# Performance work log

Hardware: AMD Instinct MI355X
Metric: run time of the kernel (lower is better)

Reference implementation:

```python
import jax, jax.numpy as jnp
import numpy as np

B = 16384

def setup_inputs() -> dict:
    key = jax.random.key(0)
    k1, k2, k3 = jax.random.split(key, 3)
    predictions = jax.random.uniform(k1, (B, 7 * 7 * 30), dtype=jnp.float32)
    targets = jax.random.uniform(k2, (B, 7 * 7 * 25), dtype=jnp.float32)
    # channel 4 of each grid cell is the object-present indicator, compared to exactly 1
    t = targets.reshape(B, 7, 7, 25)
    present = (jax.random.uniform(k3, (B, 7, 7)) > 0.5).astype(jnp.float32)
    t = t.at[..., 4].set(present)
    targets = t.reshape(B, 7 * 7 * 25)
    return {"predictions": predictions, "targets": targets}


def reference(predictions, targets):
    num_batches = predictions.shape[0]
    p = predictions.reshape(num_batches, 7, 7, 30)
    t = targets.reshape(num_batches, 7, 7, 25)

    c1 = p[..., 4]
    c2 = p[..., 9]
    c = t[..., 4]
    present = (c == 1.0)
    responsible1 = c1 > c2  # box 1 is responsible

    # objectiveness loss
    obj_present = jnp.where(responsible1, jnp.square(c1 - c), jnp.square(c2 - c))
    obj_absent = 0.5 * (jnp.square(c1) + jnp.square(c2))
    obj_loss = jnp.sum(jnp.where(present, obj_present, obj_absent))

    # classification loss (only where object present)
    cls_sq = jnp.sum(jnp.square(p[..., 10:30] - t[..., 5:25]), axis=-1)  # [B,7,7]
    class_loss = jnp.sum(jnp.where(present, cls_sq, 0.0))

    r = responsible1[..., None]
    p_center = jnp.where(r, p[..., 0:2], p[..., 5:7])
    p_hw = jnp.where(r, p[..., 2:4], p[..., 7:9])
    t_center = t[..., 0:2]
    t_hw = t[..., 2:4]
    box_sq = (jnp.sum(jnp.square(p_center - t_center), axis=-1)
              + jnp.sum(jnp.square(jnp.sqrt(p_hw) - jnp.sqrt(t_hw)), axis=-1))  # [B,7,7]
    box_loss = 5.0 * jnp.sum(jnp.where(present, box_sq, 0.0))

    return obj_loss + class_loss + box_loss
```

## Files before the change

kernel.cpp:

```cpp
#include <hip/hip_runtime.h>
#include <stdint.h>


#define TPB    64
#define KT     7
#define GRID   1792
#define P_F4   480
#define T_F4   400

#define GL2LDS(gptr, lptr)                                                    \
    __builtin_amdgcn_global_load_lds(                                         \
        (const __attribute__((address_space(1))) void*)(gptr),                \
        (__attribute__((address_space(3))) void*)(uintptr_t)(lptr), 16, 0, 0)

__global__ __launch_bounds__(TPB) void yolo_loss_kernel(
    const float* __restrict__ pred,
    const float* __restrict__ targ,
    float* __restrict__ out)
{
    __shared__ float4 spA[P_F4], stA[T_F4];
    __shared__ float4 spB[P_F4], stB[T_F4];

    const int tid = threadIdx.x;

    auto STAGE = [&](int t, float4* sp4, float4* st4) {
        const float4* gp = (const float4*)pred + (size_t)t * P_F4;
        const float4* gt = (const float4*)targ + (size_t)t * T_F4;
        #pragma unroll
        for (int r = 0; r < 7; ++r) GL2LDS(gp + tid + r * 64, sp4 + tid + r * 64);
        if (tid < 32)               GL2LDS(gp + 448 + tid,    sp4 + 448 + tid);
        #pragma unroll
        for (int r = 0; r < 6; ++r) GL2LDS(gt + tid + r * 64, st4 + tid + r * 64);
        if (tid < 16)               GL2LDS(gt + 384 + tid,    st4 + 384 + tid);
    };

    auto CELL = [&](const float* sp, const float* st) -> float {
        const float2* pv2 = (const float2*)(sp + tid * 30);
        float pv[30];
        #pragma unroll
        for (int i = 0; i < 15; ++i) {
            float2 v = pv2[i];
            pv[2*i] = v.x; pv[2*i+1] = v.y;
        }
        const float* tvp = st + tid * 25;
        float tv[25];
        #pragma unroll
        for (int i = 0; i < 25; ++i) tv[i] = tvp[i];

        float c1 = pv[4], c2 = pv[9], cc = tv[4];
        bool present = (cc == 1.0f);
        bool resp1   = (c1 > c2);

        float d1 = c1 - cc, d2 = c2 - cc;
        float obj = present ? (resp1 ? d1 * d1 : d2 * d2)
                            : 0.5f * (c1 * c1 + c2 * c2);

        float cls = 0.0f;
        #pragma unroll
        for (int k = 0; k < 20; ++k) {
            float d = pv[10 + k] - tv[5 + k];
            cls += d * d;
        }

        float pc0 = resp1 ? pv[0] : pv[5];
        float pc1 = resp1 ? pv[1] : pv[6];
        float ph0 = resp1 ? pv[2] : pv[7];
        float ph1 = resp1 ? pv[3] : pv[8];
        float b0 = pc0 - tv[0];
        float b1 = pc1 - tv[1];
        float s0 = sqrtf(ph0) - sqrtf(tv[2]);
        float s1 = sqrtf(ph1) - sqrtf(tv[3]);
        float box = b0 * b0 + b1 * b1 + s0 * s0 + s1 * s1;

        return obj + (present ? (cls + 5.0f * box) : 0.0f);
    };

    const int base = blockIdx.x * KT;
    float loss = 0.0f;

    STAGE(base, spA, stA);

    #pragma unroll
    for (int j = 0; j < KT; ++j) {
        const bool odd = (j & 1);
        if (j + 1 < KT) {
            if (odd) STAGE(base + j + 1, spA, stA);
            else     STAGE(base + j + 1, spB, stB);
            asm volatile("s_waitcnt vmcnt(15)" ::: "memory");
        } else {
            asm volatile("s_waitcnt vmcnt(0)" ::: "memory");
        }
        __builtin_amdgcn_sched_barrier(0);

        loss += odd ? CELL((const float*)spB, (const float*)stB)
                    : CELL((const float*)spA, (const float*)stA);
    }

    #pragma unroll
    for (int off = 32; off > 0; off >>= 1)
        loss += __shfl_down(loss, off);
    if (tid == 0)
        atomicAdd(out, loss);
}

extern "C" void kernel_launch(void* const* d_in, const int* in_sizes, int n_in,
                              void* d_out, int out_size, void* d_ws, size_t ws_size,
                              hipStream_t stream)
{
    const float* pred = (const float*)d_in[0];
    const float* targ = (const float*)d_in[1];
    float* out = (float*)d_out;

    hipMemsetAsync(out, 0, sizeof(float), stream);

    hipLaunchKernelGGL(yolo_loss_kernel, dim3(GRID), dim3(TPB), 0, stream,
                       pred, targ, out);
}
```

Before: 204.3 us.

## Replace LDS double-buffered staging with direct per-thread vector loads of four cells

Drops the global-to-LDS asynchronous double-buffer pipeline. Each thread now loads four contiguous grid cells straight into registers with float4 loads and computes their losses in place. Blocks grow from 64 to 256 threads on a smaller grid, with an occupancy hint added to the launch bounds. The aim is more memory-level parallelism and the removal of LDS traffic and waitcnt sequencing. In exchange, each load instruction sees strided, poorly coalesced per-lane addresses, register use rises, and there are more atomics because there are more waves.

```diff
diff --git a/kernel.cpp b/kernel.cpp
--- a/kernel.cpp
+++ b/kernel.cpp
@@ -1,105 +1,77 @@
 #include <hip/hip_runtime.h>
-#include <stdint.h>
 
 
-#define TPB    64
-#define KT     7
-#define GRID   1792
-#define P_F4   480
-#define T_F4   400
+#define TPB  256
+#define GRID 784
 
-#define GL2LDS(gptr, lptr)                                                    \
-    __builtin_amdgcn_global_load_lds(                                         \
-        (const __attribute__((address_space(1))) void*)(gptr),                \
-        (__attribute__((address_space(3))) void*)(uintptr_t)(lptr), 16, 0, 0)
+__device__ __forceinline__ float cell_loss(const float* pv, const float* tv)
+{
+    float c1 = pv[4], c2 = pv[9], cc = tv[4];
+    bool present = (cc == 1.0f);
+    bool resp1   = (c1 > c2);
 
-__global__ __launch_bounds__(TPB) void yolo_loss_kernel(
+    float d1 = c1 - cc, d2 = c2 - cc;
+    float obj = present ? (resp1 ? d1 * d1 : d2 * d2)
+                        : 0.5f * (c1 * c1 + c2 * c2);
+
+    float cls = 0.0f;
+    #pragma unroll
+    for (int k = 0; k < 20; ++k) {
+        float d = pv[10 + k] - tv[5 + k];
+        cls += d * d;
+    }
+
+    float pc0 = resp1 ? pv[0] : pv[5];
+    float pc1 = resp1 ? pv[1] : pv[6];
+    float ph0 = resp1 ? pv[2] : pv[7];
+    float ph1 = resp1 ? pv[3] : pv[8];
+    float b0 = pc0 - tv[0];
+    float b1 = pc1 - tv[1];
+    float s0 = sqrtf(ph0) - sqrtf(tv[2]);
+    float s1 = sqrtf(ph1) - sqrtf(tv[3]);
+    float box = b0 * b0 + b1 * b1 + s0 * s0 + s1 * s1;
+
+    return obj + (present ? (cls + 5.0f * box) : 0.0f);
+}
+
+__global__ __launch_bounds__(TPB, 3) void yolo_loss_kernel(
     const float* __restrict__ pred,
     const float* __restrict__ targ,
     float* __restrict__ out)
 {
-    __shared__ float4 spA[P_F4], stA[T_F4];
-    __shared__ float4 spB[P_F4], stB[T_F4];
+    const int i = blockIdx.x * TPB + threadIdx.x;
+    const float4* gp = (const float4*)pred + (size_t)i * 30;
+    const float4* gt = (const float4*)targ + (size_t)i * 25;
 
-    const int tid = threadIdx.x;
-
-    auto STAGE = [&](int t, float4* sp4, float4* st4) {
-        const float4* gp = (const float4*)pred + (size_t)t * P_F4;
-        const float4* gt = (const float4*)targ + (size_t)t * T_F4;
-        #pragma unroll
-        for (int r = 0; r < 7; ++r) GL2LDS(gp + tid + r * 64, sp4 + tid + r * 64);
-        if (tid < 32)               GL2LDS(gp + 448 + tid,    sp4 + 448 + tid);
-        #pragma unroll
-        for (int r = 0; r < 6; ++r) GL2LDS(gt + tid + r * 64, st4 + tid + r * 64);
-        if (tid < 16)               GL2LDS(gt + 384 + tid,    st4 + 384 + tid);
-    };
-
-    auto CELL = [&](const float* sp, const float* st) -> float {
-        const float2* pv2 = (const float2*)(sp + tid * 30);
-        float pv[30];
-        #pragma unroll
-        for (int i = 0; i < 15; ++i) {
-            float2 v = pv2[i];
-            pv[2*i] = v.x; pv[2*i+1] = v.y;
-        }
-        const float* tvp = st + tid * 25;
-        float tv[25];
-        #pragma unroll
-        for (int i = 0; i < 25; ++i) tv[i] = tvp[i];
-
-        float c1 = pv[4], c2 = pv[9], cc = tv[4];
-        bool present = (cc == 1.0f);
-        bool resp1   = (c1 > c2);
-
-        float d1 = c1 - cc, d2 = c2 - cc;
-        float obj = present ? (resp1 ? d1 * d1 : d2 * d2)
-                            : 0.5f * (c1 * c1 + c2 * c2);
-
-        float cls = 0.0f;
-        #pragma unroll
-        for (int k = 0; k < 20; ++k) {
-            float d = pv[10 + k] - tv[5 + k];
-            cls += d * d;
-        }
-
-        float pc0 = resp1 ? pv[0] : pv[5];
-        float pc1 = resp1 ? pv[1] : pv[6];
-        float ph0 = resp1 ? pv[2] : pv[7];
-        float ph1 = resp1 ? pv[3] : pv[8];
-        float b0 = pc0 - tv[0];
-        float b1 = pc1 - tv[1];
-        float s0 = sqrtf(ph0) - sqrtf(tv[2]);
-        float s1 = sqrtf(ph1) - sqrtf(tv[3]);
-        float box = b0 * b0 + b1 * b1 + s0 * s0 + s1 * s1;
-
-        return obj + (present ? (cls + 5.0f * box) : 0.0f);
-    };
-
-    const int base = blockIdx.x * KT;
     float loss = 0.0f;
 
-    STAGE(base, spA, stA);
-
-    #pragma unroll
-    for (int j = 0; j < KT; ++j) {
-        const bool odd = (j & 1);
-        if (j + 1 < KT) {
-            if (odd) STAGE(base + j + 1, spA, stA);
-            else     STAGE(base + j + 1, spB, stB);
-            asm volatile("s_waitcnt vmcnt(15)" ::: "memory");
-        } else {
-            asm volatile("s_waitcnt vmcnt(0)" ::: "memory");
-        }
-        __builtin_amdgcn_sched_barrier(0);
-
-        loss += odd ? CELL((const float*)spB, (const float*)stB)
-                    : CELL((const float*)spA, (const float*)stA);
+    {
+        float4 P[15], T[13];
+        #pragma unroll
+        for (int r = 0; r < 15; ++r) P[r] = gp[r];
+        #pragma unroll
+        for (int r = 0; r < 13; ++r) T[r] = gt[r];
+        const float* pv = (const float*)P;
+        const float* tv = (const float*)T;
+        loss += cell_loss(pv,      tv);
+        loss += cell_loss(pv + 30, tv + 25);
+    }
+    {
+        float4 P[15], T[13];
+        #pragma unroll
+        for (int r = 0; r < 15; ++r) P[r] = gp[15 + r];
+        #pragma unroll
+        for (int r = 0; r < 13; ++r) T[r] = gt[12 + r];
+        const float* pv = (const float*)P;
+        const float* tv = (const float*)T;
+        loss += cell_loss(pv,      tv + 2);
+        loss += cell_loss(pv + 30, tv + 27);
     }
 
     #pragma unroll
     for (int off = 32; off > 0; off >>= 1)
         loss += __shfl_down(loss, off);
-    if (tid == 0)
+    if ((threadIdx.x & 63) == 0)
         atomicAdd(out, loss);
 }
 
```

Measured after the change: 261.8 us. 1.28x slower.
